# Performance work log

Hardware: AMD Instinct MI355X
Metric: run time of the kernel (lower is better)

The kernel has to match this reference:

```python
import jax, jax.numpy as jnp
import numpy as np

N_USERS = 100000
N_ITEMS = 50000
N_NODES = N_USERS + N_ITEMS
N_EDGES = 2400000
EMB = 64
LEAKY_ALPHA = 0.3  # tf.keras.layers.LeakyReLU default


def setup_inputs() -> dict:
    key = jax.random.key(0)
    ks = jax.random.split(key, 7)
    return {
        "user_emb": jax.random.normal(ks[0], (N_USERS, EMB), dtype=jnp.float32) * 0.1,
        "item_emb": jax.random.normal(ks[1], (N_ITEMS, EMB), dtype=jnp.float32) * 0.1,
        "W0": jax.random.normal(ks[2], (EMB, EMB), dtype=jnp.float32) * (1.0 / np.sqrt(EMB)),
        "W1": jax.random.normal(ks[3], (EMB, EMB), dtype=jnp.float32) * (1.0 / np.sqrt(EMB)),
        "adj_vals": jax.random.uniform(ks[4], (N_EDGES,), dtype=jnp.float32),
        "adj_rows": jax.random.randint(ks[5], (N_EDGES,), 0, N_NODES, dtype=jnp.int32),
        "adj_cols": jax.random.randint(ks[6], (N_EDGES,), 0, N_NODES, dtype=jnp.int32),
    }


def reference(user_emb, item_emb, W0, W1, adj_vals, adj_rows, adj_cols):
    n_users = user_emb.shape[0]
    n_nodes = n_users + item_emb.shape[0]

    def spmm(e):  # sparse adjacency @ dense embeddings, COO form
        # gather source-node features, scale by edge weight, scatter-add to dest rows
        return jax.ops.segment_sum(adj_vals[:, None] * e[adj_cols], adj_rows,
                                   num_segments=n_nodes)

    e0 = jnp.concatenate([user_emb, item_emb], axis=0)          # [N, d]
    # gcn[0] = GraphConv(W0): transpose(W0 @ (A@e)^T) == (A@e) @ W0^T
    e1 = spmm(e0) @ W0.T
    # gcn[1] = LeakyReLU (Keras default alpha=0.3)
    e2 = jnp.where(e1 >= 0, e1, LEAKY_ALPHA * e1)
    # gcn[2] = GraphConv(W1)
    e3 = spmm(e2) @ W1.T
    # stack+mean over the 4 embedding stages
    all_emb = (e0 + e1 + e2 + e3) * 0.25
    return all_emb[:n_users], all_emb[n_users:]
```

## Files before the change

kernel.cpp:

```cpp
#include <hip/hip_runtime.h>

#define N_USERS 100000
#define N_ITEMS 50000
#define N_NODES 150000
#define N_EDGES 2400000
#define EMB 64
#define LEAKY 0.3f

#define RB_SHIFT 8
#define RB (1 << RB_SHIFT)
#define NBKT ((N_NODES + RB - 1) >> RB_SHIFT)
#define L1_CHUNK 16384
#define NCH ((N_EDGES + L1_CHUNK - 1) / L1_CHUNK)
#define COL_MASK 0x3FFFFu
#define NTILE (N_NODES / 16)
#define PCAP 6144

typedef unsigned short u16;
typedef unsigned int   u32;
typedef __attribute__((ext_vector_type(8))) short short8v;
typedef __attribute__((ext_vector_type(4))) float f32x4;
typedef __attribute__((ext_vector_type(2))) float v2f;

__device__ __forceinline__ u16 f32_to_bf16_rne(float f) {
    u32 u = __float_as_uint(f);
    u32 r = (u + 0x7FFFu + ((u >> 16) & 1u)) >> 16;
    return (u16)r;
}
__device__ __forceinline__ float bf16_lo(u32 x) { return __uint_as_float(x << 16); }
__device__ __forceinline__ u32 pack_bf16(float lo, float hi) {
    return (u32)f32_to_bf16_rne(lo) | ((u32)f32_to_bf16_rne(hi) << 16);
}
__device__ __forceinline__ v2f up2(u32 w) {
    v2f r;
    r.x = __uint_as_float(w << 16);
    r.y = __uint_as_float(w & 0xFFFF0000u);
    return r;
}

__global__ __launch_bounds__(1024) void conv_hist(
    const float* __restrict__ uemb, const float* __restrict__ iemb,
    const float* __restrict__ W0, const float* __restrict__ W1,
    const int* __restrict__ rows,
    u16* __restrict__ ebf, u16* __restrict__ Wbf0, u16* __restrict__ Wbf1,
    int* __restrict__ H)
{
    __shared__ int cnt[NBKT];
    const int t = threadIdx.x;
    const int b = blockIdx.x;

    if (b < NCH) {
        if (t < NBKT) cnt[t] = 0;
        __syncthreads();
        const int e0 = b * L1_CHUNK;
        const int e1 = (e0 + L1_CHUNK < N_EDGES) ? e0 + L1_CHUNK : N_EDGES;
        for (int i = e0 + t; i < e1; i += 1024)
            atomicAdd(&cnt[rows[i] >> RB_SHIFT], 1);
        __syncthreads();
        if (t < NBKT) H[b * NBKT + t] = cnt[t];
    } else {
        const int gid = (b - NCH) * 1024 + t;
        const int i = gid * 4;
        if (i < N_NODES * EMB) {
            const float* src = (i < N_USERS * EMB) ? uemb + i
                                                   : iemb + (i - N_USERS * EMB);
            const float4 v = *(const float4*)src;
            ushort4 w;
            w.x = f32_to_bf16_rne(v.x);
            w.y = f32_to_bf16_rne(v.y);
            w.z = f32_to_bf16_rne(v.z);
            w.w = f32_to_bf16_rne(v.w);
            *(ushort4*)(ebf + i) = w;
        }
        if (gid < EMB * EMB) {
            Wbf0[gid] = f32_to_bf16_rne(W0[gid]);
            Wbf1[gid] = f32_to_bf16_rne(W1[gid]);
        }
    }
}

__global__ __launch_bounds__(1024) void scan_fill(
    const int* __restrict__ H, int* __restrict__ bkt_ptr,
    int* __restrict__ B)
{
    __shared__ int lds[1024];
    const int t = threadIdx.x;

    int tot = 0;
    if (t < NBKT) {
        int a0 = 0, a1 = 0, a2 = 0, a3 = 0;
        int c = 0;
        for (; c + 4 <= NCH; c += 4) {
            a0 += H[(c + 0) * NBKT + t];
            a1 += H[(c + 1) * NBKT + t];
            a2 += H[(c + 2) * NBKT + t];
            a3 += H[(c + 3) * NBKT + t];
        }
        for (; c < NCH; ++c) a0 += H[c * NBKT + t];
        tot = (a0 + a1) + (a2 + a3);
    }
    lds[t] = (t < NBKT) ? tot : 0;
    __syncthreads();
    for (int off = 1; off < 1024; off <<= 1) {
        int x = 0;
        if (t >= off) x = lds[t - off];
        __syncthreads();
        lds[t] += x;
        __syncthreads();
    }
    const int excl = lds[t] - tot;

    if (t < NBKT) {
        bkt_ptr[t] = excl;
        int run = excl;
        int c = 0;
        for (; c + 4 <= NCH; c += 4) {
            const int h0 = H[(c + 0) * NBKT + t];
            const int h1 = H[(c + 1) * NBKT + t];
            const int h2 = H[(c + 2) * NBKT + t];
            const int h3 = H[(c + 3) * NBKT + t];
            B[(c + 0) * NBKT + t] = run;
            B[(c + 1) * NBKT + t] = run + h0;
            B[(c + 2) * NBKT + t] = run + h0 + h1;
            B[(c + 3) * NBKT + t] = run + h0 + h1 + h2;
            run += h0 + h1 + h2 + h3;
        }
        for (; c < NCH; ++c) {
            B[c * NBKT + t] = run;
            run += H[c * NBKT + t];
        }
    }
    if (t == 0) bkt_ptr[NBKT] = N_EDGES;
}

__global__ __launch_bounds__(1024) void partition_l1(
    const float* __restrict__ vals, const int* __restrict__ rows,
    const int* __restrict__ cols, const int* __restrict__ B,
    float2* __restrict__ svc)
{
    __shared__ int base[NBKT];
    __shared__ int cnt[NBKT];
    const int t = threadIdx.x;
    const int c = blockIdx.x;
    if (t < NBKT) {
        base[t] = B[c * NBKT + t];
        cnt[t]  = 0;
    }
    __syncthreads();

    const int e0 = c * L1_CHUNK;
    const int e1 = (e0 + L1_CHUNK < N_EDGES) ? e0 + L1_CHUNK : N_EDGES;
    for (int i = e0 + t; i < e1; i += 1024) {
        const int r = rows[i];
        const int b = r >> RB_SHIFT;
        const int pos = base[b] + atomicAdd(&cnt[b], 1);
        const u32 packed = ((u32)(r & (RB - 1)) << 18) | (u32)cols[i];
        svc[pos] = make_float2(vals[i], __uint_as_float(packed));
    }
}

__global__ __launch_bounds__(512) void place_l2(
    const int* __restrict__ bkt_ptr, const float2* __restrict__ svc,
    float2* __restrict__ sedge, int* __restrict__ row_ptr)
{
    __shared__ float2 E2[PCAP];
    __shared__ int cnt[RB];
    __shared__ int heads[RB];
    const int b     = blockIdx.x;
    const int rbase = b << RB_SHIFT;
    const int t     = threadIdx.x;

    if (t < RB) cnt[t] = 0;
    __syncthreads();

    const int lo = bkt_ptr[b];
    const int hi = bkt_ptr[b + 1];
    const int n  = hi - lo;

    for (int i = lo + t; i < hi; i += 512)
        atomicAdd(&cnt[__float_as_uint(svc[i].y) >> 18], 1);
    __syncthreads();

    int v = 0;
    if (t < RB) v = cnt[t];
    for (int off = 1; off < RB; off <<= 1) {
        int x = 0;
        if (t < RB && t >= off) x = cnt[t - off];
        __syncthreads();
        if (t < RB) cnt[t] += x;
        __syncthreads();
    }
    if (t < RB) {
        const int excl = cnt[t] - v;
        heads[t] = excl;
        const int gr = rbase + t;
        if (gr <= N_NODES) row_ptr[gr] = lo + excl;
    }
    __syncthreads();

    if (n <= PCAP) {
        for (int i = lo + t; i < hi; i += 512) {
            const float2 vc = svc[i];
            const int lr  = (int)(__float_as_uint(vc.y) >> 18);
            const int pos = atomicAdd(&heads[lr], 1);
            E2[pos] = vc;
        }
        __syncthreads();
        for (int i = t; i < n; i += 512)
            sedge[lo + i] = E2[i];
    } else {
        for (int i = lo + t; i < hi; i += 512) {
            const float2 vc = svc[i];
            const int lr  = (int)(__float_as_uint(vc.y) >> 18);
            const int pos = atomicAdd(&heads[lr], 1);
            sedge[lo + pos] = vc;
        }
    }
}

__global__ __launch_bounds__(256) void spmm_bf16(
    const int* __restrict__ row_ptr,
    const float2* __restrict__ sedge,
    const u16* __restrict__ ebf,
    u16* __restrict__ tbf)
{
    const int tid  = threadIdx.x;
    const int lane = tid & 63;
    const int row  = blockIdx.x * 4 + (tid >> 6);
    if (row >= N_NODES) return;

    const int g = lane >> 3;
    const int q = lane & 7;

    const int beg = row_ptr[row];
    const int end = row_ptr[row + 1];

    v2f A0 = {0.f, 0.f}, A1 = {0.f, 0.f}, A2 = {0.f, 0.f}, A3 = {0.f, 0.f};

    for (int k = beg; k < end; k += 16) {
        const int  kA  = k + g;
        const int  kB  = k + 8 + g;
        const bool onA = kA < end;
        const bool onB = kB < end;
        const float2 mA = sedge[onA ? kA : end - 1];
        const float2 mB = sedge[onB ? kB : end - 1];
        const float vA = onA ? mA.x : 0.f;
        const float vB = onB ? mB.x : 0.f;
        const u32 iA = __float_as_uint(mA.y) & COL_MASK;
        const u32 iB = __float_as_uint(mB.y) & COL_MASK;
        const uint4 xA = *((const uint4*)(ebf + (size_t)iA * EMB) + q);
        const uint4 xB = *((const uint4*)(ebf + (size_t)iB * EMB) + q);
        const v2f vvA = {vA, vA};
        const v2f vvB = {vB, vB};
        A0 = vvA * up2(xA.x) + A0;
        A1 = vvA * up2(xA.y) + A1;
        A2 = vvA * up2(xA.z) + A2;
        A3 = vvA * up2(xA.w) + A3;
        A0 = vvB * up2(xB.x) + A0;
        A1 = vvB * up2(xB.y) + A1;
        A2 = vvB * up2(xB.z) + A2;
        A3 = vvB * up2(xB.w) + A3;
    }

    float s0 = A0.x, s1 = A0.y, s2 = A1.x, s3 = A1.y;
    float s4 = A2.x, s5 = A2.y, s6 = A3.x, s7 = A3.y;
    s0 += __shfl_xor(s0, 8); s0 += __shfl_xor(s0, 16); s0 += __shfl_xor(s0, 32);
    s1 += __shfl_xor(s1, 8); s1 += __shfl_xor(s1, 16); s1 += __shfl_xor(s1, 32);
    s2 += __shfl_xor(s2, 8); s2 += __shfl_xor(s2, 16); s2 += __shfl_xor(s2, 32);
    s3 += __shfl_xor(s3, 8); s3 += __shfl_xor(s3, 16); s3 += __shfl_xor(s3, 32);
    s4 += __shfl_xor(s4, 8); s4 += __shfl_xor(s4, 16); s4 += __shfl_xor(s4, 32);
    s5 += __shfl_xor(s5, 8); s5 += __shfl_xor(s5, 16); s5 += __shfl_xor(s5, 32);
    s6 += __shfl_xor(s6, 8); s6 += __shfl_xor(s6, 16); s6 += __shfl_xor(s6, 32);
    s7 += __shfl_xor(s7, 8); s7 += __shfl_xor(s7, 16); s7 += __shfl_xor(s7, 32);

    if (g == 0) {
        uint4 w;
        w.x = pack_bf16(s0, s1);
        w.y = pack_bf16(s2, s3);
        w.z = pack_bf16(s4, s5);
        w.w = pack_bf16(s6, s7);
        *(uint4*)(tbf + (size_t)row * EMB + 8 * q) = w;
    }
}

template <bool FIRST>
__global__ __launch_bounds__(256) void dense_mfma(
    const u16* __restrict__ tbf,
    const u16* __restrict__ Wbf,
    u16* ebf,
    u16* __restrict__ obf,
    float* __restrict__ out)
{
    const int tid  = threadIdx.x;
    const int l    = tid & 63;
    const int tile = blockIdx.x * 4 + (tid >> 6);
    if (tile >= NTILE) return;
    const int row0 = tile * 16;

    const int lr = l & 15;
    const int lk = l >> 4;

    short8v bfrag[4][2];
    #pragma unroll
    for (int c = 0; c < 4; ++c)
        #pragma unroll
        for (int kh = 0; kh < 2; ++kh)
            bfrag[c][kh] = *(const short8v*)(Wbf + (size_t)(16 * c + lr) * EMB
                                             + 32 * kh + 8 * lk);

    const u16* trow = tbf + (size_t)(row0 + lr) * EMB;
    const short8v afrag0 = *(const short8v*)(trow + 8 * lk);
    const short8v afrag1 = *(const short8v*)(trow + 32 + 8 * lk);

    f32x4 acc[4];
    #pragma unroll
    for (int c = 0; c < 4; ++c) {
        f32x4 z = {0.f, 0.f, 0.f, 0.f};
        z = __builtin_amdgcn_mfma_f32_16x16x32_bf16(afrag0, bfrag[c][0], z, 0, 0, 0);
        z = __builtin_amdgcn_mfma_f32_16x16x32_bf16(afrag1, bfrag[c][1], z, 0, 0, 0);
        acc[c] = z;
    }

    #pragma unroll
    for (int c = 0; c < 4; ++c) {
        #pragma unroll
        for (int r = 0; r < 4; ++r) {
            const int row = row0 + 4 * lk + r;
            const size_t idx = (size_t)row * EMB + 16 * c + lr;
            const float e1v = acc[c][r];
            if (FIRST) {
                const float e2v = (e1v >= 0.f) ? e1v : LEAKY * e1v;
                const float e0v = bf16_lo((u32)ebf[idx]);
                obf[idx] = f32_to_bf16_rne(0.25f * (e0v + e1v + e2v));
                ebf[idx] = f32_to_bf16_rne(e2v);
            } else {
                out[idx] = bf16_lo((u32)obf[idx]) + 0.25f * e1v;
            }
        }
    }
}

__global__ __launch_bounds__(256) void spmm_atomic(
    const float* __restrict__ vals, const int* __restrict__ rows,
    const int* __restrict__ cols, const float* __restrict__ src_a,
    const float* __restrict__ src_b, float* __restrict__ dst)
{
    const int tid  = threadIdx.x;
    const int lane = tid & 63;
    const int e    = blockIdx.x * 4 + (tid >> 6);
    if (e >= N_EDGES) return;
    const float v = vals[e];
    const int   c = cols[e];
    const int   r = rows[e];
    const float* src = (src_b != nullptr && c >= N_USERS)
                           ? src_b + (size_t)(c - N_USERS) * EMB
                           : src_a + (size_t)c * EMB;
    unsafeAtomicAdd(&dst[(size_t)r * EMB + lane], v * src[lane]);
}

template <bool FIRST>
__global__ __launch_bounds__(256) void dense_f32(
    const float* __restrict__ t, const float* __restrict__ W,
    const float* __restrict__ user_emb, const float* __restrict__ item_emb,
    float* __restrict__ e2, float* __restrict__ out)
{
    __shared__ float wT[64][65];
    __shared__ float trow[16][64];

    const int tid = threadIdx.x;
    for (int k = tid; k < 64 * 64; k += 256) {
        const int i = k >> 6, j = k & 63;
        wT[j][i] = W[k];
    }
    const int row_base = blockIdx.x * 16;
    for (int k = tid; k < 16 * 64; k += 256) {
        const int r = k >> 6, j = k & 63;
        const int row = row_base + r;
        trow[r][j] = (row < N_NODES) ? t[(size_t)row * EMB + j] : 0.f;
    }
    __syncthreads();

    const int i  = tid & 63;
    const int r0 = tid >> 6;

    #pragma unroll
    for (int rr = 0; rr < 4; ++rr) {
        const int r   = r0 * 4 + rr;
        const int row = row_base + r;
        if (row >= N_NODES) continue;
        float acc = 0.f;
        #pragma unroll
        for (int j = 0; j < 64; ++j)
            acc = fmaf(trow[r][j], wT[j][i], acc);
        const size_t idx = (size_t)row * EMB + i;
        if (FIRST) {
            const float e1v = acc;
            const float e2v = (e1v >= 0.f) ? e1v : LEAKY * e1v;
            const float e0v = (row < N_USERS)
                                  ? user_emb[idx]
                                  : item_emb[(size_t)(row - N_USERS) * EMB + i];
            e2[idx]  = e2v;
            out[idx] = 0.25f * (e0v + e1v + e2v);
        } else {
            out[idx] += 0.25f * acc;
        }
    }
}

extern "C" void kernel_launch(void* const* d_in, const int* in_sizes, int n_in,
                              void* d_out, int out_size, void* d_ws, size_t ws_size,
                              hipStream_t stream)
{
    const float* user_emb = (const float*)d_in[0];
    const float* item_emb = (const float*)d_in[1];
    const float* W0       = (const float*)d_in[2];
    const float* W1       = (const float*)d_in[3];
    const float* adj_vals = (const float*)d_in[4];
    const int*   adj_rows = (const int*)d_in[5];
    const int*   adj_cols = (const int*)d_in[6];
    float*       out      = (float*)d_out;

    const size_t mat_bytes = (size_t)N_NODES * EMB * sizeof(float);
    const size_t ebf_bytes = (size_t)N_NODES * EMB * sizeof(u16);
    const size_t edge8     = (size_t)N_EDGES * sizeof(float2);
    const size_t hmat      = (size_t)NCH * NBKT * sizeof(int);

    const size_t off_tbf    = 0;
    const size_t off_svc    = 0;
    const size_t off_sedge  = off_tbf + ebf_bytes;
    const size_t off_ebf    = off_sedge + edge8;
    const size_t off_obf    = off_ebf + ebf_bytes;
    const size_t off_rowptr = off_obf + ebf_bytes;
    const size_t off_H      = off_rowptr + (size_t)(N_NODES + 1) * sizeof(int);
    const size_t off_B      = off_H + hmat;
    const size_t off_ptr    = off_B + hmat;
    const size_t off_wbf    = (off_ptr + (size_t)(NBKT + 1) * sizeof(int) + 15) & ~(size_t)15;
    const size_t required   = off_wbf + 2 * (size_t)EMB * EMB * sizeof(u16);

    const int spmm_blocks   = (N_NODES + 3) / 4;
    const int densem_blocks = (NTILE + 3) / 4;
    const int convh_blocks  = NCH + (N_NODES * EMB / 4 + 1023) / 1024;

    if (ws_size >= required) {
        u16*    tbf     = (u16*)((char*)d_ws + off_tbf);
        float2* svc     = (float2*)((char*)d_ws + off_svc);
        float2* sedge   = (float2*)((char*)d_ws + off_sedge);
        u16*    ebf     = (u16*)((char*)d_ws + off_ebf);
        u16*    obf     = (u16*)((char*)d_ws + off_obf);
        int*    row_ptr = (int*)((char*)d_ws + off_rowptr);
        int*    H       = (int*)((char*)d_ws + off_H);
        int*    B       = (int*)((char*)d_ws + off_B);
        int*    bkt_ptr = (int*)((char*)d_ws + off_ptr);
        u16*    Wbf0    = (u16*)((char*)d_ws + off_wbf);
        u16*    Wbf1    = Wbf0 + EMB * EMB;

        conv_hist<<<convh_blocks, 1024, 0, stream>>>(
            user_emb, item_emb, W0, W1, adj_rows, ebf, Wbf0, Wbf1, H);

        scan_fill<<<1, 1024, 0, stream>>>(H, bkt_ptr, B);
        partition_l1<<<NCH, 1024, 0, stream>>>(
            adj_vals, adj_rows, adj_cols, B, svc);
        place_l2<<<NBKT, 512, 0, stream>>>(bkt_ptr, svc, sedge, row_ptr);

        spmm_bf16<<<spmm_blocks, 256, 0, stream>>>(row_ptr, sedge, ebf, tbf);
        dense_mfma<true><<<densem_blocks, 256, 0, stream>>>(
            tbf, Wbf0, ebf, obf, out);

        spmm_bf16<<<spmm_blocks, 256, 0, stream>>>(row_ptr, sedge, ebf, tbf);
        dense_mfma<false><<<densem_blocks, 256, 0, stream>>>(
            tbf, Wbf1, ebf, obf, out);
    } else {
        float* t  = (float*)d_ws;
        float* e2 = (float*)((char*)d_ws + mat_bytes);
        const int dense_blocks = (N_NODES + 15) / 16;

        hipMemsetAsync(t, 0, mat_bytes, stream);
        spmm_atomic<<<(N_EDGES + 3) / 4, 256, 0, stream>>>(
            adj_vals, adj_rows, adj_cols, user_emb, item_emb, t);
        dense_f32<true><<<dense_blocks, 256, 0, stream>>>(
            t, W0, user_emb, item_emb, e2, out);

        hipMemsetAsync(t, 0, mat_bytes, stream);
        spmm_atomic<<<(N_EDGES + 3) / 4, 256, 0, stream>>>(
            adj_vals, adj_rows, adj_cols, e2, nullptr, t);
        dense_f32<false><<<dense_blocks, 256, 0, stream>>>(
            t, W1, nullptr, nullptr, nullptr, out);
    }
}
```

Measured before the change: 209.2 us.

## Fuse SpMM aggregation with MFMA dense transform per 16-row tile

Merges the gather-based SpMM kernel and the MFMA dense kernel into one kernel per layer. Each block aggregates 16 rows into shared memory, then each wave computes one 16-column slice of the 64x64 transform and applies the epilogue. This removes the bf16 intermediate round trip through global memory and two kernel launches. In exchange it adds a block barrier, each wave now handles 4 rows serially, and e2 goes to a separate buffer that reuses the partition scratch region to avoid a read/write race.

```diff
diff --git a/kernel.cpp b/kernel.cpp
--- a/kernel.cpp
+++ b/kernel.cpp
@@ -218,124 +218,107 @@
     }
 }
 
-__global__ __launch_bounds__(256) void spmm_bf16(
+template <bool FIRST>
+__global__ __launch_bounds__(256) void fused_stage(
     const int* __restrict__ row_ptr,
     const float2* __restrict__ sedge,
+    const u16* __restrict__ src,
+    const u16* __restrict__ Wbf,
     const u16* __restrict__ ebf,
-    u16* __restrict__ tbf)
-{
+    u16* __restrict__ e2bf,
+    u16* __restrict__ obf,
+    float* __restrict__ out)
+{
+    __shared__ u16 trow[16][72];
+
     const int tid  = threadIdx.x;
     const int lane = tid & 63;
-    const int row  = blockIdx.x * 4 + (tid >> 6);
-    if (row >= N_NODES) return;
+    const int w    = tid >> 6;
+    const int row0 = blockIdx.x * 16;
 
     const int g = lane >> 3;
     const int q = lane & 7;
 
-    const int beg = row_ptr[row];
-    const int end = row_ptr[row + 1];
-
-    v2f A0 = {0.f, 0.f}, A1 = {0.f, 0.f}, A2 = {0.f, 0.f}, A3 = {0.f, 0.f};
-
-    for (int k = beg; k < end; k += 16) {
-        const int  kA  = k + g;
-        const int  kB  = k + 8 + g;
-        const bool onA = kA < end;
-        const bool onB = kB < end;
-        const float2 mA = sedge[onA ? kA : end - 1];
-        const float2 mB = sedge[onB ? kB : end - 1];
-        const float vA = onA ? mA.x : 0.f;
-        const float vB = onB ? mB.x : 0.f;
-        const u32 iA = __float_as_uint(mA.y) & COL_MASK;
-        const u32 iB = __float_as_uint(mB.y) & COL_MASK;
-        const uint4 xA = *((const uint4*)(ebf + (size_t)iA * EMB) + q);
-        const uint4 xB = *((const uint4*)(ebf + (size_t)iB * EMB) + q);
-        const v2f vvA = {vA, vA};
-        const v2f vvB = {vB, vB};
-        A0 = vvA * up2(xA.x) + A0;
-        A1 = vvA * up2(xA.y) + A1;
-        A2 = vvA * up2(xA.z) + A2;
-        A3 = vvA * up2(xA.w) + A3;
-        A0 = vvB * up2(xB.x) + A0;
-        A1 = vvB * up2(xB.y) + A1;
-        A2 = vvB * up2(xB.z) + A2;
-        A3 = vvB * up2(xB.w) + A3;
-    }
-
-    float s0 = A0.x, s1 = A0.y, s2 = A1.x, s3 = A1.y;
-    float s4 = A2.x, s5 = A2.y, s6 = A3.x, s7 = A3.y;
-    s0 += __shfl_xor(s0, 8); s0 += __shfl_xor(s0, 16); s0 += __shfl_xor(s0, 32);
-    s1 += __shfl_xor(s1, 8); s1 += __shfl_xor(s1, 16); s1 += __shfl_xor(s1, 32);
-    s2 += __shfl_xor(s2, 8); s2 += __shfl_xor(s2, 16); s2 += __shfl_xor(s2, 32);
-    s3 += __shfl_xor(s3, 8); s3 += __shfl_xor(s3, 16); s3 += __shfl_xor(s3, 32);
-    s4 += __shfl_xor(s4, 8); s4 += __shfl_xor(s4, 16); s4 += __shfl_xor(s4, 32);
-    s5 += __shfl_xor(s5, 8); s5 += __shfl_xor(s5, 16); s5 += __shfl_xor(s5, 32);
-    s6 += __shfl_xor(s6, 8); s6 += __shfl_xor(s6, 16); s6 += __shfl_xor(s6, 32);
-    s7 += __shfl_xor(s7, 8); s7 += __shfl_xor(s7, 16); s7 += __shfl_xor(s7, 32);
-
-    if (g == 0) {
-        uint4 w;
-        w.x = pack_bf16(s0, s1);
-        w.y = pack_bf16(s2, s3);
-        w.z = pack_bf16(s4, s5);
-        w.w = pack_bf16(s6, s7);
-        *(uint4*)(tbf + (size_t)row * EMB + 8 * q) = w;
-    }
-}
-
-template <bool FIRST>
-__global__ __launch_bounds__(256) void dense_mfma(
-    const u16* __restrict__ tbf,
-    const u16* __restrict__ Wbf,
-    u16* ebf,
-    u16* __restrict__ obf,
-    float* __restrict__ out)
-{
-    const int tid  = threadIdx.x;
-    const int l    = tid & 63;
-    const int tile = blockIdx.x * 4 + (tid >> 6);
-    if (tile >= NTILE) return;
-    const int row0 = tile * 16;
-
-    const int lr = l & 15;
-    const int lk = l >> 4;
-
-    short8v bfrag[4][2];
     #pragma unroll
-    for (int c = 0; c < 4; ++c)
-        #pragma unroll
-        for (int kh = 0; kh < 2; ++kh)
-            bfrag[c][kh] = *(const short8v*)(Wbf + (size_t)(16 * c + lr) * EMB
-                                             + 32 * kh + 8 * lk);
-
-    const u16* trow = tbf + (size_t)(row0 + lr) * EMB;
-    const short8v afrag0 = *(const short8v*)(trow + 8 * lk);
-    const short8v afrag1 = *(const short8v*)(trow + 32 + 8 * lk);
-
-    f32x4 acc[4];
+    for (int rr = 0; rr < 4; ++rr) {
+        const int tr  = 4 * w + rr;
+        const int row = row0 + tr;
+        const int beg = row_ptr[row];
+        const int end = row_ptr[row + 1];
+
+        v2f A0 = {0.f, 0.f}, A1 = {0.f, 0.f}, A2 = {0.f, 0.f}, A3 = {0.f, 0.f};
+
+        for (int k = beg; k < end; k += 16) {
+            const int  kA  = k + g;
+            const int  kB  = k + 8 + g;
+            const bool onA = kA < end;
+            const bool onB = kB < end;
+            const float2 mA = sedge[onA ? kA : end - 1];
+            const float2 mB = sedge[onB ? kB : end - 1];
+            const float vA = onA ? mA.x : 0.f;
+            const float vB = onB ? mB.x : 0.f;
+            const u32 iA = __float_as_uint(mA.y) & COL_MASK;
+            const u32 iB = __float_as_uint(mB.y) & COL_MASK;
+            const uint4 xA = *((const uint4*)(src + (size_t)iA * EMB) + q);
+            const uint4 xB = *((const uint4*)(src + (size_t)iB * EMB) + q);
+            const v2f vvA = {vA, vA};
+            const v2f vvB = {vB, vB};
+            A0 = vvA * up2(xA.x) + A0;
+            A1 = vvA * up2(xA.y) + A1;
+            A2 = vvA * up2(xA.z) + A2;
+            A3 = vvA * up2(xA.w) + A3;
+            A0 = vvB * up2(xB.x) + A0;
+            A1 = vvB * up2(xB.y) + A1;
+            A2 = vvB * up2(xB.z) + A2;
+            A3 = vvB * up2(xB.w) + A3;
+        }
+
+        float s0 = A0.x, s1 = A0.y, s2 = A1.x, s3 = A1.y;
+        float s4 = A2.x, s5 = A2.y, s6 = A3.x, s7 = A3.y;
+        s0 += __shfl_xor(s0, 8); s0 += __shfl_xor(s0, 16); s0 += __shfl_xor(s0, 32);
+        s1 += __shfl_xor(s1, 8); s1 += __shfl_xor(s1, 16); s1 += __shfl_xor(s1, 32);
+        s2 += __shfl_xor(s2, 8); s2 += __shfl_xor(s2, 16); s2 += __shfl_xor(s2, 32);
+        s3 += __shfl_xor(s3, 8); s3 += __shfl_xor(s3, 16); s3 += __shfl_xor(s3, 32);
+        s4 += __shfl_xor(s4, 8); s4 += __shfl_xor(s4, 16); s4 += __shfl_xor(s4, 32);
+        s5 += __shfl_xor(s5, 8); s5 += __shfl_xor(s5, 16); s5 += __shfl_xor(s5, 32);
+        s6 += __shfl_xor(s6, 8); s6 += __shfl_xor(s6, 16); s6 += __shfl_xor(s6, 32);
+        s7 += __shfl_xor(s7, 8); s7 += __shfl_xor(s7, 16); s7 += __shfl_xor(s7, 32);
+
+        if (g == 0) {
+            uint4 wv;
+            wv.x = pack_bf16(s0, s1);
+            wv.y = pack_bf16(s2, s3);
+            wv.z = pack_bf16(s4, s5);
+            wv.w = pack_bf16(s6, s7);
+            *(uint4*)(&trow[tr][8 * q]) = wv;
+        }
+    }
+    __syncthreads();
+
+    const int lr = lane & 15;
+    const int lk = lane >> 4;
+
+    const short8v bfrag0 = *(const short8v*)(Wbf + (size_t)(16 * w + lr) * EMB + 8 * lk);
+    const short8v bfrag1 = *(const short8v*)(Wbf + (size_t)(16 * w + lr) * EMB + 32 + 8 * lk);
+    const short8v afrag0 = *(const short8v*)(&trow[lr][8 * lk]);
+    const short8v afrag1 = *(const short8v*)(&trow[lr][32 + 8 * lk]);
+
+    f32x4 acc = {0.f, 0.f, 0.f, 0.f};
+    acc = __builtin_amdgcn_mfma_f32_16x16x32_bf16(afrag0, bfrag0, acc, 0, 0, 0);
+    acc = __builtin_amdgcn_mfma_f32_16x16x32_bf16(afrag1, bfrag1, acc, 0, 0, 0);
+
     #pragma unroll
-    for (int c = 0; c < 4; ++c) {
-        f32x4 z = {0.f, 0.f, 0.f, 0.f};
-        z = __builtin_amdgcn_mfma_f32_16x16x32_bf16(afrag0, bfrag[c][0], z, 0, 0, 0);
-        z = __builtin_amdgcn_mfma_f32_16x16x32_bf16(afrag1, bfrag[c][1], z, 0, 0, 0);
-        acc[c] = z;
-    }
-
-    #pragma unroll
-    for (int c = 0; c < 4; ++c) {
-        #pragma unroll
-        for (int r = 0; r < 4; ++r) {
-            const int row = row0 + 4 * lk + r;
-            const size_t idx = (size_t)row * EMB + 16 * c + lr;
-            const float e1v = acc[c][r];
-            if (FIRST) {
-                const float e2v = (e1v >= 0.f) ? e1v : LEAKY * e1v;
-                const float e0v = bf16_lo((u32)ebf[idx]);
-                obf[idx] = f32_to_bf16_rne(0.25f * (e0v + e1v + e2v));
-                ebf[idx] = f32_to_bf16_rne(e2v);
-            } else {
-                out[idx] = bf16_lo((u32)obf[idx]) + 0.25f * e1v;
-            }
+    for (int r = 0; r < 4; ++r) {
+        const int row = row0 + 4 * lk + r;
+        const size_t idx = (size_t)row * EMB + 16 * w + lr;
+        const float e1v = acc[r];
+        if (FIRST) {
+            const float e2v = (e1v >= 0.f) ? e1v : LEAKY * e1v;
+            const float e0v = bf16_lo((u32)ebf[idx]);
+            obf[idx]  = f32_to_bf16_rne(0.25f * (e0v + e1v + e2v));
+            e2bf[idx] = f32_to_bf16_rne(e2v);
+        } else {
+            out[idx] = bf16_lo((u32)obf[idx]) + 0.25f * e1v;
         }
     }
 }
@@ -425,9 +408,8 @@
     const size_t edge8     = (size_t)N_EDGES * sizeof(float2);
     const size_t hmat      = (size_t)NCH * NBKT * sizeof(int);
 
-    const size_t off_tbf    = 0;
     const size_t off_svc    = 0;
-    const size_t off_sedge  = off_tbf + ebf_bytes;
+    const size_t off_sedge  = off_svc + edge8;
     const size_t off_ebf    = off_sedge + edge8;
     const size_t off_obf    = off_ebf + ebf_bytes;
     const size_t off_rowptr = off_obf + ebf_bytes;
@@ -437,13 +419,11 @@
     const size_t off_wbf    = (off_ptr + (size_t)(NBKT + 1) * sizeof(int) + 15) & ~(size_t)15;
     const size_t required   = off_wbf + 2 * (size_t)EMB * EMB * sizeof(u16);
 
-    const int spmm_blocks   = (N_NODES + 3) / 4;
-    const int densem_blocks = (NTILE + 3) / 4;
     const int convh_blocks  = NCH + (N_NODES * EMB / 4 + 1023) / 1024;
 
     if (ws_size >= required) {
-        u16*    tbf     = (u16*)((char*)d_ws + off_tbf);
         float2* svc     = (float2*)((char*)d_ws + off_svc);
+        u16*    e2bf    = (u16*)((char*)d_ws + off_svc);
         float2* sedge   = (float2*)((char*)d_ws + off_sedge);
         u16*    ebf     = (u16*)((char*)d_ws + off_ebf);
         u16*    obf     = (u16*)((char*)d_ws + off_obf);
@@ -462,13 +442,11 @@
             adj_vals, adj_rows, adj_cols, B, svc);
         place_l2<<<NBKT, 512, 0, stream>>>(bkt_ptr, svc, sedge, row_ptr);
 
-        spmm_bf16<<<spmm_blocks, 256, 0, stream>>>(row_ptr, sedge, ebf, tbf);
-        dense_mfma<true><<<densem_blocks, 256, 0, stream>>>(
-            tbf, Wbf0, ebf, obf, out);
-
-        spmm_bf16<<<spmm_blocks, 256, 0, stream>>>(row_ptr, sedge, ebf, tbf);
-        dense_mfma<false><<<densem_blocks, 256, 0, stream>>>(
-            tbf, Wbf1, ebf, obf, out);
+        fused_stage<true><<<NTILE, 256, 0, stream>>>(
+            row_ptr, sedge, ebf, Wbf0, ebf, e2bf, obf, out);
+
+        fused_stage<false><<<NTILE, 256, 0, stream>>>(
+            row_ptr, sedge, e2bf, Wbf1, nullptr, nullptr, obf, out);
     } else {
         float* t  = (float*)d_ws;
         float* e2 = (float*)((char*)d_ws + mat_bytes);
```

After: 185.4 us. 1.13x faster.
